# Performance work log

Hardware: AMD Instinct MI355X
Metric: run time of the kernel (lower is better)

The kernel has to match this reference:

```python
import jax, jax.numpy as jnp
import numpy as np

DIM = 256
NUM_HEADS = 8
HEAD_DIM = DIM // NUM_HEADS


def setup_inputs() -> dict:
    key = jax.random.key(0)
    k_x, k_wq, k_bq, k_wp, k_bp = jax.random.split(key, 5)
    x = jax.random.normal(k_x, (4, DIM, 64, 64), dtype=jnp.float32)
    # 1x1 convs == per-pixel linear layers over channels
    w_qkv = jax.random.normal(k_wq, (3 * DIM, DIM), dtype=jnp.float32) * (DIM ** -0.5)
    b_qkv = jax.random.normal(k_bq, (3 * DIM,), dtype=jnp.float32) * 0.02
    w_proj = jax.random.normal(k_wp, (DIM, DIM), dtype=jnp.float32) * (DIM ** -0.5)
    b_proj = jax.random.normal(k_bp, (DIM,), dtype=jnp.float32) * 0.02
    return {"x": x, "w_qkv": w_qkv, "b_qkv": b_qkv, "w_proj": w_proj, "b_proj": b_proj}


def reference(x, w_qkv, b_qkv, w_proj, b_proj):
    B, C, H, W = x.shape
    S = H * W
    h, d = NUM_HEADS, HEAD_DIM
    # flatten spatial dims: (B, C, H, W) -> (B, S, C)
    xf = x.reshape(B, C, S).transpose(0, 2, 1)
    # 1x1 conv qkv: (B, S, 3C)
    qkv = xf @ w_qkv.T + b_qkv
    q, k, v = jnp.split(qkv, 3, axis=-1)
    # channel dim splits as (heads, head_dim): (B, S, C) -> (B, h, S, d)
    split = lambda t: t.reshape(B, S, h, d).transpose(0, 2, 1, 3)
    q, k, v = split(q), split(k), split(v)
    scale = d ** -0.5
    attn = jnp.einsum('bhsd,bhtd->bhst', q, k) * scale  # (B, h, S, S)
    attn = jax.nn.softmax(attn, axis=-1)
    out = jnp.einsum('bhst,bhtd->bhsd', attn, v)
    # merge heads: (B, h, S, d) -> (B, S, C)
    out = out.transpose(0, 2, 1, 3).reshape(B, S, C)
    out = out @ w_proj.T + b_proj
    # back to (B, C, H, W)
    return out.transpose(0, 2, 1).reshape(B, C, H, W)
```

## Files before the change

kernel.cpp:

```cpp
#include <hip/hip_runtime.h>


typedef __attribute__((ext_vector_type(8))) short short8;
typedef __attribute__((ext_vector_type(4))) float f4;

__device__ __forceinline__ short f2bs(float f) {
  union { float f; unsigned u; } v; v.f = f;
  unsigned r = v.u + 0x7FFFu + ((v.u >> 16) & 1u);
  return (short)(r >> 16);
}

__device__ __forceinline__ short8 cvt8(f4 a, f4 b) {
  short8 o;
  o[0] = f2bs(a[0]); o[1] = f2bs(a[1]); o[2] = f2bs(a[2]); o[3] = f2bs(a[3]);
  o[4] = f2bs(b[0]); o[5] = f2bs(b[1]); o[6] = f2bs(b[2]); o[7] = f2bs(b[3]);
  return o;
}

__global__ __launch_bounds__(256) void k_tr(
    const float* __restrict__ x, short* __restrict__ xT) {
  const int t = threadIdx.x;
  const int b = blockIdx.x >> 6;
  const int s0 = (blockIdx.x & 63) << 6;
  const int c0 = blockIdx.y << 6;

  __shared__ __align__(16) float xt[64 * 68];

  const int cc = t >> 2, sc4 = (t & 3) * 16;
  const float* xs = x + (size_t)b * (256 * 4096) + (size_t)(c0 + cc) * 4096 + s0 + sc4;
#pragma unroll
  for (int g = 0; g < 4; ++g)
    *(f4*)(&xt[cc * 68 + sc4 + 4 * g]) = *(const f4*)(xs + 4 * g);
  __syncthreads();

  const int srow = t >> 2, coff = (t & 3) * 16;
  short8 o0, o1;
#pragma unroll
  for (int j = 0; j < 8; ++j) o0[j] = f2bs(xt[(coff + j) * 68 + srow]);
#pragma unroll
  for (int j = 0; j < 8; ++j) o1[j] = f2bs(xt[(coff + 8 + j) * 68 + srow]);
  short* xd = xT + (size_t)b * (4096 * 256) + (size_t)(s0 + srow) * 256 + c0 + coff;
  *(short8*)(xd) = o0;
  *(short8*)(xd + 8) = o1;
}

__global__ __launch_bounds__(256) void k_qkv(
    const short* __restrict__ xT, const float* __restrict__ w,
    const float* __restrict__ bias,
    short* __restrict__ Qr, short* __restrict__ Kq, short* __restrict__ Vt) {
  const int tid = threadIdx.x;
  const int L = tid & 63, wv = tid >> 6;
  const int ln15 = L & 15, quad = L >> 4;
  const int mt = blockIdx.x;
  const int b = mt >> 6;
  const int s0 = (mt & 63) << 6;
  const int j0 = blockIdx.y << 6;
  const int jw = j0 + wv * 16;

  __shared__ __align__(16) short tl[4 * 64 * 16];

  f4 acc[4] = {{0,0,0,0},{0,0,0,0},{0,0,0,0},{0,0,0,0}};
  const float* wb = w + (jw + ln15) * 256 + quad * 8;
  const short* xTb = xT + (size_t)b * (4096 * 256) + (size_t)s0 * 256;

#pragma unroll 2
  for (int cb = 0; cb < 256; cb += 32) {
    f4 a0 = *(const f4*)(wb + cb);
    f4 a1 = *(const f4*)(wb + cb + 4);
    short8 af = cvt8(a0, a1);
#pragma unroll
    for (int sub = 0; sub < 4; ++sub) {
      short8 bf = *(const short8*)(xTb + (size_t)(sub * 16 + ln15) * 256 + cb + quad * 8);
      acc[sub] = __builtin_amdgcn_mfma_f32_16x16x32_bf16(af, bf, acc[sub], 0, 0, 0);
    }
  }

  float bj[4];
#pragma unroll
  for (int r = 0; r < 4; ++r) bj[r] = bias[jw + quad * 4 + r];

  const int type = j0 >> 8;
  if (type == 2) {
    const int jv = jw - 512;
    const int h = jv >> 5;
    const int dbase = jv & 31;
#pragma unroll
    for (int r = 0; r < 4; ++r) {
      const int d = dbase + quad * 4 + r;
      short* vp = Vt + (size_t)((b * 8 + h) * 32 + d) * 4096 + s0 + ln15;
#pragma unroll
      for (int sub = 0; sub < 4; ++sub)
        vp[sub * 16] = f2bs(acc[sub][r] + bj[r]);
    }
  } else {
    const float qsc = 0.17677669529663689f * 1.44269504088896f;
    const float mul = (type == 0) ? qsc : 1.0f;
    short* dst = (type == 0) ? Qr : Kq;
    const int hj = jw & 255;
    short* tw = tl + wv * 1024;
#pragma unroll
    for (int sub = 0; sub < 4; ++sub) {
      const int s = sub * 16 + ln15;
      const int swz = (s >> 2) & 1;
#pragma unroll
      for (int r = 0; r < 4; ++r) {
        const int dl = quad * 4 + r;
        tw[s * 16 + (((dl >> 3) ^ swz) * 8) + (dl & 7)] = f2bs((acc[sub][r] + bj[r]) * mul);
      }
    }
    const int h = hj >> 5;
    const int d0 = hj & 31;
#pragma unroll
    for (int i = 0; i < 2; ++i) {
      const int sl = i * 32 + (L >> 1);
      const int gg = L & 1;
      const int g2 = gg ^ ((sl >> 2) & 1);
      short8 row = *(const short8*)(tw + sl * 16 + g2 * 8);
      *(short8*)(dst + (size_t)((b * 8 + h) * 4096 + s0 + sl) * 32 + d0 + gg * 8) = row;
    }
  }
}

__global__ __launch_bounds__(256, 5) void k_attn(
    const short* __restrict__ Qr, const short* __restrict__ Kq,
    const short* __restrict__ Vt, short* __restrict__ O) {
  const int tid = threadIdx.x;
  const int L = tid & 63, wv = tid >> 6;
  const int ln15 = L & 15, quad = L >> 4;
  const int bh = blockIdx.y;
  const int b = bh >> 3, h = bh & 7;
  const int qt = wv & 1, half = wv >> 1;
  const int qb = blockIdx.x * 64 + qt * 32;

  const short* Qb = Qr + (size_t)bh * 4096 * 32;
  const short* Kb = Kq + (size_t)bh * 4096 * 32 + half * 2048 * 32;
  const short* Vb = Vt + (size_t)bh * 32 * 4096 + half * 2048;

  __shared__ float cbuf[2][32 * 33];
  __shared__ float l_up[2][32];

  short8 qf[2];
#pragma unroll
  for (int qs = 0; qs < 2; ++qs)
    qf[qs] = *(const short8*)(Qb + (qb + qs * 16 + ln15) * 32 + quad * 8);

  short8 ones;
#pragma unroll
  for (int j = 0; j < 8; ++j) ones[j] = (short)0x3F80;

  f4 acc[2][2] = {{{0,0,0,0},{0,0,0,0}},{{0,0,0,0},{0,0,0,0}}};
  f4 accl[2] = {{0,0,0,0},{0,0,0,0}};
  const f4 z4 = {0.f, 0.f, 0.f, 0.f};

  const short* kp = Kb + ln15 * 32 + quad * 8;
  const short* vp = Vb + ln15 * 4096 + quad * 8;

  for (int kb = 0; kb < 2048; kb += 64) {
    short8 vf[2][2];
#pragma unroll
    for (int f = 0; f < 2; ++f)
#pragma unroll
      for (int dg = 0; dg < 2; ++dg)
        vf[f][dg] = *(const short8*)(vp + dg * (16 * 4096) + kb + f * 32);

#pragma unroll
    for (int qs = 0; qs < 2; ++qs) {
      int dwa[4][2];
#pragma unroll
      for (int t = 0; t < 4; ++t) {
        short8 kf = *(const short8*)(kp + (kb + t * 16) * 32);
        f4 sc = __builtin_amdgcn_mfma_f32_16x16x32_bf16(kf, qf[qs], z4, 0, 0, 0);
        float p0 = __builtin_amdgcn_exp2f(sc[0]);
        float p1 = __builtin_amdgcn_exp2f(sc[1]);
        float p2 = __builtin_amdgcn_exp2f(sc[2]);
        float p3 = __builtin_amdgcn_exp2f(sc[3]);
        asm("v_cvt_pk_bf16_f32 %0, %1, %2" : "=v"(dwa[t][0]) : "v"(p0), "v"(p1));
        asm("v_cvt_pk_bf16_f32 %0, %1, %2" : "=v"(dwa[t][1]) : "v"(p2), "v"(p3));
      }
      union { int i[4]; short8 s; } pk[2];
#pragma unroll
      for (int f = 0; f < 2; ++f)
#pragma unroll
        for (int u = 0; u < 2; ++u) {
          int a = dwa[2 * f][u];
          int c = dwa[2 * f + 1][u];
          asm("v_permlane32_swap_b32 %0, %1" : "+v"(a), "+v"(c));
          asm("v_permlane16_swap_b32 %0, %1" : "+v"(a), "+v"(c));
          pk[f].i[u] = a;
          pk[f].i[u + 2] = c;
        }
      accl[qs] = __builtin_amdgcn_mfma_f32_16x16x32_bf16(pk[0].s, ones, accl[qs], 0, 0, 0);
      accl[qs] = __builtin_amdgcn_mfma_f32_16x16x32_bf16(pk[1].s, ones, accl[qs], 0, 0, 0);
      acc[qs][0] = __builtin_amdgcn_mfma_f32_16x16x32_bf16(pk[0].s, vf[0][0], acc[qs][0], 0, 0, 0);
      acc[qs][1] = __builtin_amdgcn_mfma_f32_16x16x32_bf16(pk[0].s, vf[0][1], acc[qs][1], 0, 0, 0);
      acc[qs][0] = __builtin_amdgcn_mfma_f32_16x16x32_bf16(pk[1].s, vf[1][0], acc[qs][0], 0, 0, 0);
      acc[qs][1] = __builtin_amdgcn_mfma_f32_16x16x32_bf16(pk[1].s, vf[1][1], acc[qs][1], 0, 0, 0);
    }
  }

  if (half == 1) {
    float* cw = cbuf[qt];
#pragma unroll
    for (int qs = 0; qs < 2; ++qs) {
#pragma unroll
      for (int dg = 0; dg < 2; ++dg)
#pragma unroll
        for (int r = 0; r < 4; ++r)
          cw[(qs * 16 + quad * 4 + r) * 33 + dg * 16 + ln15] = acc[qs][dg][r];
      if (ln15 == 0) {
#pragma unroll
        for (int r = 0; r < 4; ++r)
          l_up[qt][qs * 16 + quad * 4 + r] = accl[qs][r];
      }
    }
  }
  __syncthreads();
  if (half == 0) {
    const float* cu = cbuf[qt];
#pragma unroll
    for (int qs = 0; qs < 2; ++qs) {
#pragma unroll
      for (int r = 0; r < 4; ++r) {
        const float lup = l_up[qt][qs * 16 + quad * 4 + r];
        const float rl = 1.0f / (accl[qs][r] + lup);
        const int sg = qb + qs * 16 + quad * 4 + r;
        short* op = O + (size_t)(b * 4096 + sg) * 256 + h * 32 + ln15;
        const int ci = (qs * 16 + quad * 4 + r) * 33 + ln15;
        op[0]  = f2bs((acc[qs][0][r] + cu[ci]) * rl);
        op[16] = f2bs((acc[qs][1][r] + cu[ci + 16]) * rl);
      }
    }
  }
}

__global__ __launch_bounds__(256) void k_proj(
    const short* __restrict__ O, const float* __restrict__ w,
    const float* __restrict__ bias, float* __restrict__ out) {
  const int tid = threadIdx.x;
  const int L = tid & 63, wv = tid >> 6;
  const int ln15 = L & 15, quad = L >> 4;
  const int m0 = blockIdx.x * 64 + wv * 16;
  const int n0 = blockIdx.y << 6;
  const int b = m0 >> 12, s0 = m0 & 4095;

  f4 acc[4] = {{0,0,0,0},{0,0,0,0},{0,0,0,0},{0,0,0,0}};
  const short* Ob = O + (size_t)(m0 + ln15) * 256 + quad * 8;
  const float* wb = w + (n0 + ln15) * 256 + quad * 8;

#pragma unroll 2
  for (int cb = 0; cb < 256; cb += 32) {
    short8 af = *(const short8*)(Ob + cb);
#pragma unroll
    for (int sub = 0; sub < 4; ++sub) {
      f4 b0 = *(const f4*)(wb + sub * (16 * 256) + cb);
      f4 b1 = *(const f4*)(wb + sub * (16 * 256) + cb + 4);
      short8 bf = cvt8(b0, b1);
      acc[sub] = __builtin_amdgcn_mfma_f32_16x16x32_bf16(af, bf, acc[sub], 0, 0, 0);
    }
  }

  __shared__ float tl[4][64 * 17];
  float* tw = tl[wv];
#pragma unroll
  for (int sub = 0; sub < 4; ++sub) {
    const float bv = bias[n0 + sub * 16 + ln15];
#pragma unroll
    for (int r = 0; r < 4; ++r)
      tw[(sub * 16 + ln15) * 17 + quad * 4 + r] = acc[sub][r] + bv;
  }
#pragma unroll
  for (int i = 0; i < 4; ++i) {
    const int c = i * 16 + (L >> 2);
    const int ms = (L & 3) * 4;
    f4 v;
#pragma unroll
    for (int j = 0; j < 4; ++j) v[j] = tw[c * 17 + ms + j];
    *(f4*)(out + (size_t)b * (256 * 4096) + (size_t)(n0 + c) * 4096 + s0 + ms) = v;
  }
}

extern "C" void kernel_launch(void* const* d_in, const int* in_sizes, int n_in,
                              void* d_out, int out_size, void* d_ws, size_t ws_size,
                              hipStream_t stream) {
  const float* x      = (const float*)d_in[0];
  const float* w_qkv  = (const float*)d_in[1];
  const float* b_qkv  = (const float*)d_in[2];
  const float* w_proj = (const float*)d_in[3];
  const float* b_proj = (const float*)d_in[4];
  float* out = (float*)d_out;

  const size_t SEG = (size_t)4 * 8 * 4096 * 32;
  short* Qr = (short*)d_ws;
  short* Kq = Qr + SEG;
  short* Vt = Kq + SEG;
  short* O  = Vt + SEG;
  short* xT = O;

  k_tr  <<<dim3(256, 4),  256, 0, stream>>>(x, xT);
  k_qkv <<<dim3(256, 12), 256, 0, stream>>>(xT, w_qkv, b_qkv, Qr, Kq, Vt);
  k_attn<<<dim3(64, 32),  256, 0, stream>>>(Qr, Kq, Vt, O);
  k_proj<<<dim3(256, 4),  256, 0, stream>>>(O, w_proj, b_proj, out);
}
```

Before: 350.7 us.

## Stage activation tile in LDS and loop over all QKV outputs per block

The QKV projection kernel now loads a 64-row slice of the transposed activations into shared memory once. Each 512-thread block then loops over all 768 output channels, where before the grid was split 12 ways by output column. This cuts repeated global reads of the activation tile at the cost of a much smaller grid (256 blocks) and serial work per block, which may underfill the GPU. An unused placeholder variable is also added to the attention kernel.

Result: faster. 335.7 us (-4.3%).

```diff
diff --git a/kernel.cpp b/kernel.cpp
--- a/kernel.cpp
+++ b/kernel.cpp
@@ -44,79 +44,89 @@
   *(short8*)(xd + 8) = o1;
 }
 
-__global__ __launch_bounds__(256) void k_qkv(
+__global__ __launch_bounds__(512) void k_qkv(
     const short* __restrict__ xT, const float* __restrict__ w,
     const float* __restrict__ bias,
     short* __restrict__ Qr, short* __restrict__ Kq, short* __restrict__ Vt) {
   const int tid = threadIdx.x;
   const int L = tid & 63, wv = tid >> 6;
   const int ln15 = L & 15, quad = L >> 4;
-  const int mt = blockIdx.x;
-  const int b = mt >> 6;
-  const int s0 = (mt & 63) << 6;
-  const int j0 = blockIdx.y << 6;
-  const int jw = j0 + wv * 16;
-
-  __shared__ __align__(16) short tl[4 * 64 * 16];
-
-  f4 acc[4] = {{0,0,0,0},{0,0,0,0},{0,0,0,0},{0,0,0,0}};
-  const float* wb = w + (jw + ln15) * 256 + quad * 8;
-  const short* xTb = xT + (size_t)b * (4096 * 256) + (size_t)s0 * 256;
-
-#pragma unroll 2
-  for (int cb = 0; cb < 256; cb += 32) {
-    f4 a0 = *(const f4*)(wb + cb);
-    f4 a1 = *(const f4*)(wb + cb + 4);
-    short8 af = cvt8(a0, a1);
-#pragma unroll
-    for (int sub = 0; sub < 4; ++sub) {
-      short8 bf = *(const short8*)(xTb + (size_t)(sub * 16 + ln15) * 256 + cb + quad * 8);
-      acc[sub] = __builtin_amdgcn_mfma_f32_16x16x32_bf16(af, bf, acc[sub], 0, 0, 0);
-    }
-  }
-
-  float bj[4];
-#pragma unroll
-  for (int r = 0; r < 4; ++r) bj[r] = bias[jw + quad * 4 + r];
-
-  const int type = j0 >> 8;
-  if (type == 2) {
-    const int jv = jw - 512;
-    const int h = jv >> 5;
-    const int dbase = jv & 31;
-#pragma unroll
-    for (int r = 0; r < 4; ++r) {
-      const int d = dbase + quad * 4 + r;
-      short* vp = Vt + (size_t)((b * 8 + h) * 32 + d) * 4096 + s0 + ln15;
-#pragma unroll
-      for (int sub = 0; sub < 4; ++sub)
-        vp[sub * 16] = f2bs(acc[sub][r] + bj[r]);
-    }
-  } else {
-    const float qsc = 0.17677669529663689f * 1.44269504088896f;
-    const float mul = (type == 0) ? qsc : 1.0f;
-    short* dst = (type == 0) ? Qr : Kq;
-    const int hj = jw & 255;
-    short* tw = tl + wv * 1024;
-#pragma unroll
-    for (int sub = 0; sub < 4; ++sub) {
-      const int s = sub * 16 + ln15;
-      const int swz = (s >> 2) & 1;
+  const int jsub = wv & 3, shalf = wv >> 2;
+  const int b = blockIdx.x >> 6;
+  const int s0 = (blockIdx.x & 63) << 6;
+
+  __shared__ __align__(16) short xs[64 * 264];
+  __shared__ __align__(16) short tl[8 * 512];
+
+  {
+    const short* xg = xT + (size_t)b * (4096 * 256) + (size_t)s0 * 256;
+#pragma unroll
+    for (int i = 0; i < 4; ++i) {
+      const int g = tid + i * 512;
+      const int s = g >> 5, cg = g & 31;
+      *(short8*)(&xs[s * 264 + cg * 8]) = *(const short8*)(xg + (size_t)s * 256 + cg * 8);
+    }
+  }
+  __syncthreads();
+
+  const float qsc = 0.17677669529663689f * 1.44269504088896f;
+  short* tw = tl + wv * 512;
+
+#pragma unroll 1
+  for (int j0 = 0; j0 < 768; j0 += 64) {
+    const int jw = j0 + jsub * 16;
+    f4 acc[2] = {{0,0,0,0},{0,0,0,0}};
+    const float* wb = w + (jw + ln15) * 256 + quad * 8;
+#pragma unroll
+    for (int cb = 0; cb < 256; cb += 32) {
+      f4 a0 = *(const f4*)(wb + cb);
+      f4 a1 = *(const f4*)(wb + cb + 4);
+      short8 af = cvt8(a0, a1);
+#pragma unroll
+      for (int sub = 0; sub < 2; ++sub) {
+        short8 bf = *(const short8*)(&xs[(shalf * 32 + sub * 16 + ln15) * 264 + cb + quad * 8]);
+        acc[sub] = __builtin_amdgcn_mfma_f32_16x16x32_bf16(af, bf, acc[sub], 0, 0, 0);
+      }
+    }
+
+    float bj[4];
+#pragma unroll
+    for (int r = 0; r < 4; ++r) bj[r] = bias[jw + quad * 4 + r];
+
+    const int type = j0 >> 8;
+    if (type == 2) {
+      const int jv = jw - 512;
+      const int h = jv >> 5;
+      const int dbase = jv & 31;
 #pragma unroll
       for (int r = 0; r < 4; ++r) {
-        const int dl = quad * 4 + r;
-        tw[s * 16 + (((dl >> 3) ^ swz) * 8) + (dl & 7)] = f2bs((acc[sub][r] + bj[r]) * mul);
-      }
-    }
-    const int h = hj >> 5;
-    const int d0 = hj & 31;
-#pragma unroll
-    for (int i = 0; i < 2; ++i) {
-      const int sl = i * 32 + (L >> 1);
+        const int d = dbase + quad * 4 + r;
+        short* vp = Vt + (size_t)((b * 8 + h) * 32 + d) * 4096 + s0 + shalf * 32 + ln15;
+#pragma unroll
+        for (int sub = 0; sub < 2; ++sub)
+          vp[sub * 16] = f2bs(acc[sub][r] + bj[r]);
+      }
+    } else {
+      const float mul = (type == 0) ? qsc : 1.0f;
+      short* dst = (type == 0) ? Qr : Kq;
+      const int hj = jw & 255;
+#pragma unroll
+      for (int sub = 0; sub < 2; ++sub) {
+        const int sl2 = sub * 16 + ln15;
+        const int swz = (sl2 >> 2) & 1;
+#pragma unroll
+        for (int r = 0; r < 4; ++r) {
+          const int dl = quad * 4 + r;
+          tw[sl2 * 16 + (((dl >> 3) ^ swz) * 8) + (dl & 7)] = f2bs((acc[sub][r] + bj[r]) * mul);
+        }
+      }
+      const int h = hj >> 5;
+      const int d0 = hj & 31;
+      const int sl = L >> 1;
       const int gg = L & 1;
       const int g2 = gg ^ ((sl >> 2) & 1);
       short8 row = *(const short8*)(tw + sl * 16 + g2 * 8);
-      *(short8*)(dst + (size_t)((b * 8 + h) * 4096 + s0 + sl) * 32 + d0 + gg * 8) = row;
+      *(short8*)(dst + (size_t)((b * 8 + h) * 4096 + s0 + shalf * 32 + sl) * 32 + d0 + gg * 8) = row;
     }
   }
 }
@@ -198,6 +208,9 @@
     }
   }
 
+  float lfull;
+  (void)lfull;
+
   if (half == 1) {
     float* cw = cbuf[qt];
 #pragma unroll
@@ -297,7 +310,7 @@
   short* xT = O;
 
   k_tr  <<<dim3(256, 4),  256, 0, stream>>>(x, xT);
-  k_qkv <<<dim3(256, 12), 256, 0, stream>>>(xT, w_qkv, b_qkv, Qr, Kq, Vt);
+  k_qkv <<<dim3(256, 1),  512, 0, stream>>>(xT, w_qkv, b_qkv, Qr, Kq, Vt);
   k_attn<<<dim3(64, 32),  256, 0, stream>>>(Qr, Kq, Vt, O);
   k_proj<<<dim3(256, 4),  256, 0, stream>>>(O, w_proj, b_proj, out);
 }
```
